# Kernel optimization log

Measured on AMD Instinct MI355X. Metric: run time of the kernel, lower is better.

The kernel has to match this reference:

```python
import jax, jax.numpy as jnp
import numpy as np

B, H, W = 8, 1024, 1024
DIM = 33  # LUT resolution per axis


def identity_lut(dim=DIM):
    # lut[0, b, g, r] = r/(dim-1); lut[1, b, g, r] = g/(dim-1); lut[2, b, g, r] = b/(dim-1)
    coords = jnp.arange(dim, dtype=jnp.float32) / (dim - 1)
    r = jnp.broadcast_to(coords[None, None, :], (dim, dim, dim))
    g = jnp.broadcast_to(coords[None, :, None], (dim, dim, dim))
    b = jnp.broadcast_to(coords[:, None, None], (dim, dim, dim))
    return jnp.stack([r, g, b], axis=0)  # [3, dim, dim, dim]


def setup_inputs() -> dict:
    key = jax.random.key(0)
    x = jax.random.uniform(key, (B, 3, H, W), dtype=jnp.float32)  # RGB in [0,1)
    lut = identity_lut(DIM)  # learned parameter, identity init as in the module
    return {"lut": lut, "x": x}


def _trilinear_lut_apply(lut, x):
    # lut: [3, dim, dim, dim] indexed as [channel, b, g, r]; x: [B, 3, H, W] in [0,1]
    dim = lut.shape[1]
    scale = jnp.float32(dim - 1)
    r = x[:, 0] * scale  # [B, H, W]
    g = x[:, 1] * scale
    b = x[:, 2] * scale

    ir = jnp.clip(jnp.floor(r).astype(jnp.int32), 0, dim - 2)
    ig = jnp.clip(jnp.floor(g).astype(jnp.int32), 0, dim - 2)
    ib = jnp.clip(jnp.floor(b).astype(jnp.int32), 0, dim - 2)

    fr = r - ir.astype(x.dtype)
    fg = g - ig.astype(x.dtype)
    fb = b - ib.astype(x.dtype)

    lut_flat = lut.reshape(3, dim * dim * dim)  # [3, dim^3]
    base = (ib * dim + ig) * dim + ir  # flat index of (b,g,r) corner, [B,H,W]

    out = jnp.zeros_like(x)  # [B, 3, H, W]
    for db in (0, 1):
        wb = fb if db else (1.0 - fb)
        for dg in (0, 1):
            wg = fg if dg else (1.0 - fg)
            for dr in (0, 1):
                wr = fr if dr else (1.0 - fr)
                idx = base + (db * dim + dg) * dim + dr  # [B,H,W]
                corner = lut_flat[:, idx]  # gather -> [3, B, H, W]
                w = (wb * wg * wr)[None]  # [1, B, H, W]
                out = out + jnp.transpose(corner * w, (1, 0, 2, 3))
    return out


def reference(lut, x):
    return _trilinear_lut_apply(lut, x)
```

## Files before the change

kernel.cpp:

```cpp
#include <hip/hip_runtime.h>
#include <math.h>

typedef float        f32x4 __attribute__((ext_vector_type(4)));
typedef unsigned int u32x4 __attribute__((ext_vector_type(4)));

static constexpr int DIM    = 33;
static constexpr int LUT_N  = DIM * DIM * DIM;
static constexpr int HW     = 1024 * 1024;
static constexpr int BATCH  = 8;
static constexpr long NPIX  = (long)BATCH * HW;
static constexpr long NTASK = NPIX / 4;

static constexpr size_t QT_BYTES  = (size_t)LUT_N * 4;
static constexpr size_t MM_OFF    = 143872;
static constexpr size_t LDS_BYTES = QT_BYTES;

static constexpr int ABLK = 256;
static constexpr int ATHR = 1024;

__device__ __forceinline__ f32x4 ntl4(const float* p) {
    return __builtin_nontemporal_load((const f32x4*)p);
}
__device__ __forceinline__ void nts4(float* p, f32x4 v) {
    __builtin_nontemporal_store(v, (f32x4*)p);
}
__device__ __forceinline__ float d_r(unsigned n) { return (float)(n & 1023u); }
__device__ __forceinline__ float d_g(unsigned n) { return (float)((n >> 10) & 1023u); }
__device__ __forceinline__ float d_b(unsigned n) { return (float)(n >> 20); }

__global__ __launch_bounds__(1024) void lut_minmax(
    const float* __restrict__ lut, float* __restrict__ mm) {
    __shared__ float smin[1024], smax[1024];
    int t = threadIdx.x;
    float vmin = 1e30f, vmax = -1e30f;
    const f32x4* l4 = (const f32x4*)lut;
    const int NV = (3 * LUT_N) / 4;
#pragma unroll 4
    for (int i = t; i < NV; i += 1024) {
        f32x4 v = l4[i];
        vmin = fminf(vmin, fminf(fminf(v[0], v[1]), fminf(v[2], v[3])));
        vmax = fmaxf(vmax, fmaxf(fmaxf(v[0], v[1]), fmaxf(v[2], v[3])));
    }
    if (t < 3) {
        float v = lut[NV * 4 + t];
        vmin = fminf(vmin, v);
        vmax = fmaxf(vmax, v);
    }
    smin[t] = vmin; smax[t] = vmax;
    __syncthreads();
    for (int s = 512; s > 0; s >>= 1) {
        if (t < s) {
            smin[t] = fminf(smin[t], smin[t + s]);
            smax[t] = fmaxf(smax[t], smax[t + s]);
        }
        __syncthreads();
    }
    if (t == 0) { mm[0] = smin[0]; mm[1] = smax[0]; }
}

__global__ __launch_bounds__(256) void repack_u10(
    const float* __restrict__ lut, unsigned* __restrict__ qt,
    const float* __restrict__ mm) {
    int i = blockIdx.x * 256 + threadIdx.x;
    if (i >= LUT_N) return;
    float mn = mm[0], mx = mm[1];
    float range = mx - mn;
    if (range < 1e-20f) range = 1e-20f;
    float scale = 1023.0f / range;
    unsigned qr = (unsigned)__float2int_rn((lut[i] - mn) * scale);
    unsigned qg = (unsigned)__float2int_rn((lut[LUT_N + i] - mn) * scale);
    unsigned qb = (unsigned)__float2int_rn((lut[2 * LUT_N + i] - mn) * scale);
    qt[i] = qr | (qg << 10) | (qb << 20);
}

__global__ __launch_bounds__(1024) void lut_apply_lds(
    const float* __restrict__ x, const unsigned* __restrict__ qt,
    const float* __restrict__ mm, float* __restrict__ out) {
    extern __shared__ unsigned sl[];
    {
        const u32x4* q4 = (const u32x4*)qt;
        u32x4* s4 = (u32x4*)sl;
#pragma unroll
        for (int k = 0; k < 9; ++k) {
            int i = threadIdx.x + k * 1024;
            if (i < LUT_N / 4) s4[i] = q4[i];
        }
        if (threadIdx.x == 0) sl[LUT_N - 1] = qt[LUT_N - 1];
    }
    float mn = mm[0];
    float range = mm[1] - mn;
    if (range < 1e-20f) range = 1e-20f;
    float inv = range * (1.0f / 1023.0f);
    __syncthreads();

    const int gtid = blockIdx.x * ATHR + threadIdx.x;
    const size_t hw4 = (size_t)gtid * 4;
    const float* xp = x + hw4;
    float*       op = out + hw4;

    f32x4 rc = ntl4(xp);
    f32x4 gc = ntl4(xp + HW);
    f32x4 bc = ntl4(xp + 2 * (size_t)HW);

    for (int it = 0; it < BATCH; ++it) {
        f32x4 rn = {}, gn = {}, bn = {};
        if (it != BATCH - 1) {
            const float* xn = xp + (size_t)(it + 1) * (3 * (size_t)HW);
            rn = ntl4(xn);
            gn = ntl4(xn + HW);
            bn = ntl4(xn + 2 * (size_t)HW);
        }

        unsigned n[4][8];
        float fr[4], fg[4], fb[4];
#pragma unroll
        for (int i = 0; i < 4; ++i) {
            const float scale = (float)(DIM - 1);
            float rs = rc[i] * scale, gs = gc[i] * scale, bs = bc[i] * scale;
            int ir = (int)rs; ir = ir < 0 ? 0 : (ir > DIM - 2 ? DIM - 2 : ir);
            int ig = (int)gs; ig = ig < 0 ? 0 : (ig > DIM - 2 ? DIM - 2 : ig);
            int ib = (int)bs; ib = ib < 0 ? 0 : (ib > DIM - 2 ? DIM - 2 : ib);
            fr[i] = rs - (float)ir;
            fg[i] = gs - (float)ig;
            fb[i] = bs - (float)ib;
            int s = ib * (DIM * DIM) + ig * DIM + ir;
            n[i][0] = sl[s];                     n[i][1] = sl[s + 1];
            n[i][2] = sl[s + DIM];               n[i][3] = sl[s + DIM + 1];
            n[i][4] = sl[s + DIM * DIM];         n[i][5] = sl[s + DIM * DIM + 1];
            n[i][6] = sl[s + DIM * DIM + DIM];   n[i][7] = sl[s + DIM * DIM + DIM + 1];
        }

        f32x4 orv, ogv, obv;
#pragma unroll
        for (int i = 0; i < 4; ++i) {
            float frc = 1.0f - fr[i], fgc = 1.0f - fg[i], fbc = 1.0f - fb[i];
            float w00 = fbc * fgc, w01 = fbc * fg[i];
            float w10 = fb[i] * fgc, w11 = fb[i] * fg[i];
            float u0 = w00 * frc, u1 = w00 * fr[i];
            float u2 = w01 * frc, u3 = w01 * fr[i];
            float u4 = w10 * frc, u5 = w10 * fr[i];
            float u6 = w11 * frc, u7 = w11 * fr[i];

            float qr = u0 * d_r(n[i][0]);
            qr = fmaf(u1, d_r(n[i][1]), qr);
            qr = fmaf(u2, d_r(n[i][2]), qr);
            qr = fmaf(u3, d_r(n[i][3]), qr);
            qr = fmaf(u4, d_r(n[i][4]), qr);
            qr = fmaf(u5, d_r(n[i][5]), qr);
            qr = fmaf(u6, d_r(n[i][6]), qr);
            qr = fmaf(u7, d_r(n[i][7]), qr);

            float qg = u0 * d_g(n[i][0]);
            qg = fmaf(u1, d_g(n[i][1]), qg);
            qg = fmaf(u2, d_g(n[i][2]), qg);
            qg = fmaf(u3, d_g(n[i][3]), qg);
            qg = fmaf(u4, d_g(n[i][4]), qg);
            qg = fmaf(u5, d_g(n[i][5]), qg);
            qg = fmaf(u6, d_g(n[i][6]), qg);
            qg = fmaf(u7, d_g(n[i][7]), qg);

            float qb = u0 * d_b(n[i][0]);
            qb = fmaf(u1, d_b(n[i][1]), qb);
            qb = fmaf(u2, d_b(n[i][2]), qb);
            qb = fmaf(u3, d_b(n[i][3]), qb);
            qb = fmaf(u4, d_b(n[i][4]), qb);
            qb = fmaf(u5, d_b(n[i][5]), qb);
            qb = fmaf(u6, d_b(n[i][6]), qb);
            qb = fmaf(u7, d_b(n[i][7]), qb);

            orv[i] = fmaf(qr, inv, mn);
            ogv[i] = fmaf(qg, inv, mn);
            obv[i] = fmaf(qb, inv, mn);
        }

        float* o = op + (size_t)it * (3 * (size_t)HW);
        nts4(o, orv);
        nts4(o + HW, ogv);
        nts4(o + 2 * (size_t)HW, obv);

        rc = rn; gc = gn; bc = bn;
    }
}

__global__ __launch_bounds__(256) void lut_apply_soa(
    const float* __restrict__ x, const float* __restrict__ lut,
    float* __restrict__ out) {
    long t = (long)blockIdx.x * 256 + threadIdx.x;
    long p = t * 4;
    int  b  = (int)(p >> 20);
    int  hw = (int)(p & (HW - 1));
    size_t base = (size_t)b * (3 * (size_t)HW) + (size_t)hw;

    float4 rv = *(const float4*)(x + base);
    float4 gv = *(const float4*)(x + base + (size_t)HW);
    float4 bv = *(const float4*)(x + base + 2 * (size_t)HW);

    float rr[4] = {rv.x, rv.y, rv.z, rv.w};
    float gg[4] = {gv.x, gv.y, gv.z, gv.w};
    float bb[4] = {bv.x, bv.y, bv.z, bv.w};
    float orr[4], org[4], orb[4];

#pragma unroll
    for (int i = 0; i < 4; ++i) {
        const float scale = (float)(DIM - 1);
        float rs = rr[i] * scale, gs = gg[i] * scale, bs = bb[i] * scale;
        int ir = (int)floorf(rs); ir = ir < 0 ? 0 : (ir > DIM - 2 ? DIM - 2 : ir);
        int ig = (int)floorf(gs); ig = ig < 0 ? 0 : (ig > DIM - 2 ? DIM - 2 : ig);
        int ib = (int)floorf(bs); ib = ib < 0 ? 0 : (ib > DIM - 2 ? DIM - 2 : ib);
        float fr = rs - (float)ir, fg = gs - (float)ig, fb = bs - (float)ib;
        int base_i = (ib * DIM + ig) * DIM + ir;
        float acc[3] = {0.f, 0.f, 0.f};
#pragma unroll
        for (int db = 0; db < 2; ++db) {
            float wb = db ? fb : 1.f - fb;
#pragma unroll
            for (int dg = 0; dg < 2; ++dg) {
                float wg = dg ? fg : 1.f - fg;
#pragma unroll
                for (int dr = 0; dr < 2; ++dr) {
                    float wr = dr ? fr : 1.f - fr;
                    int idx = base_i + (db * DIM + dg) * DIM + dr;
                    float w = wb * wg * wr;
                    acc[0] = fmaf(w, lut[idx], acc[0]);
                    acc[1] = fmaf(w, lut[LUT_N + idx], acc[1]);
                    acc[2] = fmaf(w, lut[2 * LUT_N + idx], acc[2]);
                }
            }
        }
        orr[i] = acc[0]; org[i] = acc[1]; orb[i] = acc[2];
    }

    *(float4*)(out + base)                  = make_float4(orr[0], orr[1], orr[2], orr[3]);
    *(float4*)(out + base + (size_t)HW)     = make_float4(org[0], org[1], org[2], org[3]);
    *(float4*)(out + base + 2 * (size_t)HW) = make_float4(orb[0], orb[1], orb[2], orb[3]);
}

extern "C" void kernel_launch(void* const* d_in, const int* in_sizes, int n_in,
                              void* d_out, int out_size, void* d_ws, size_t ws_size,
                              hipStream_t stream) {
    const float* lut = (const float*)d_in[0];
    const float* x   = (const float*)d_in[1];
    if (n_in >= 2 && in_sizes[0] > in_sizes[1]) {
        lut = (const float*)d_in[1];
        x   = (const float*)d_in[0];
    }
    float* out = (float*)d_out;

    const size_t need = MM_OFF + 2 * sizeof(float);
    if (ws_size >= need) {
        unsigned* qt = (unsigned*)d_ws;
        float*    mm = (float*)((char*)d_ws + MM_OFF);
        (void)hipFuncSetAttribute((const void*)lut_apply_lds,
                                  hipFuncAttributeMaxDynamicSharedMemorySize,
                                  (int)LDS_BYTES);
        lut_minmax<<<1, 1024, 0, stream>>>(lut, mm);
        repack_u10<<<(LUT_N + 255) / 256, 256, 0, stream>>>(lut, qt, mm);
        lut_apply_lds<<<ABLK, ATHR, LDS_BYTES, stream>>>(x, qt, mm, out);
    } else {
        lut_apply_soa<<<(int)(NTASK / 256), 256, 0, stream>>>(x, lut, out);
    }
}
```

Before: 189.3 us.

## Fuse LUT min/max, quantize-repack, and apply into a single kernel

```diff
diff --git a/kernel.cpp b/kernel.cpp
--- a/kernel.cpp
+++ b/kernel.cpp
@@ -12,8 +12,7 @@
 static constexpr long NTASK = NPIX / 4;
 
 static constexpr size_t QT_BYTES  = (size_t)LUT_N * 4;
-static constexpr size_t MM_OFF    = 143872;
-static constexpr size_t LDS_BYTES = QT_BYTES;
+static constexpr size_t LDS_BYTES = 143872;
 
 static constexpr int ABLK = 256;
 static constexpr int ATHR = 1024;
@@ -28,72 +27,59 @@
 __device__ __forceinline__ float d_g(unsigned n) { return (float)((n >> 10) & 1023u); }
 __device__ __forceinline__ float d_b(unsigned n) { return (float)(n >> 20); }
 
-__global__ __launch_bounds__(1024) void lut_minmax(
-    const float* __restrict__ lut, float* __restrict__ mm) {
-    __shared__ float smin[1024], smax[1024];
-    int t = threadIdx.x;
+__global__ __launch_bounds__(1024) void lut_fused(
+    const float* __restrict__ x, const float* __restrict__ lut,
+    float* __restrict__ out) {
+    extern __shared__ unsigned sl[];
+    const int t = threadIdx.x;
+
     float vmin = 1e30f, vmax = -1e30f;
-    const f32x4* l4 = (const f32x4*)lut;
-    const int NV = (3 * LUT_N) / 4;
+    {
+        const f32x4* l4 = (const f32x4*)lut;
+        const int NV = (3 * LUT_N) / 4;
 #pragma unroll 4
-    for (int i = t; i < NV; i += 1024) {
-        f32x4 v = l4[i];
-        vmin = fminf(vmin, fminf(fminf(v[0], v[1]), fminf(v[2], v[3])));
-        vmax = fmaxf(vmax, fmaxf(fmaxf(v[0], v[1]), fmaxf(v[2], v[3])));
-    }
-    if (t < 3) {
-        float v = lut[NV * 4 + t];
-        vmin = fminf(vmin, v);
-        vmax = fmaxf(vmax, v);
-    }
-    smin[t] = vmin; smax[t] = vmax;
+        for (int i = t; i < NV; i += 1024) {
+            f32x4 v = l4[i];
+            vmin = fminf(vmin, fminf(fminf(v[0], v[1]), fminf(v[2], v[3])));
+            vmax = fmaxf(vmax, fmaxf(fmaxf(v[0], v[1]), fmaxf(v[2], v[3])));
+        }
+        if (t < 3) {
+            float v = lut[NV * 4 + t];
+            vmin = fminf(vmin, v);
+            vmax = fmaxf(vmax, v);
+        }
+    }
+#pragma unroll
+    for (int off = 32; off > 0; off >>= 1) {
+        vmin = fminf(vmin, __shfl_down(vmin, off));
+        vmax = fmaxf(vmax, __shfl_down(vmax, off));
+    }
+    float* sf = (float*)sl;
+    if ((t & 63) == 0) { sf[t >> 6] = vmin; sf[16 + (t >> 6)] = vmax; }
     __syncthreads();
-    for (int s = 512; s > 0; s >>= 1) {
-        if (t < s) {
-            smin[t] = fminf(smin[t], smin[t + s]);
-            smax[t] = fmaxf(smax[t], smax[t + s]);
-        }
-        __syncthreads();
-    }
-    if (t == 0) { mm[0] = smin[0]; mm[1] = smax[0]; }
-}
-
-__global__ __launch_bounds__(256) void repack_u10(
-    const float* __restrict__ lut, unsigned* __restrict__ qt,
-    const float* __restrict__ mm) {
-    int i = blockIdx.x * 256 + threadIdx.x;
-    if (i >= LUT_N) return;
-    float mn = mm[0], mx = mm[1];
+    float mn = sf[0], mx = sf[16];
+#pragma unroll
+    for (int k = 1; k < 16; ++k) {
+        mn = fminf(mn, sf[k]);
+        mx = fmaxf(mx, sf[16 + k]);
+    }
+    __syncthreads();
+
     float range = mx - mn;
     if (range < 1e-20f) range = 1e-20f;
-    float scale = 1023.0f / range;
-    unsigned qr = (unsigned)__float2int_rn((lut[i] - mn) * scale);
-    unsigned qg = (unsigned)__float2int_rn((lut[LUT_N + i] - mn) * scale);
-    unsigned qb = (unsigned)__float2int_rn((lut[2 * LUT_N + i] - mn) * scale);
-    qt[i] = qr | (qg << 10) | (qb << 20);
-}
-
-__global__ __launch_bounds__(1024) void lut_apply_lds(
-    const float* __restrict__ x, const unsigned* __restrict__ qt,
-    const float* __restrict__ mm, float* __restrict__ out) {
-    extern __shared__ unsigned sl[];
-    {
-        const u32x4* q4 = (const u32x4*)qt;
-        u32x4* s4 = (u32x4*)sl;
-#pragma unroll
-        for (int k = 0; k < 9; ++k) {
-            int i = threadIdx.x + k * 1024;
-            if (i < LUT_N / 4) s4[i] = q4[i];
-        }
-        if (threadIdx.x == 0) sl[LUT_N - 1] = qt[LUT_N - 1];
-    }
-    float mn = mm[0];
-    float range = mm[1] - mn;
-    if (range < 1e-20f) range = 1e-20f;
-    float inv = range * (1.0f / 1023.0f);
+    const float qscale = 1023.0f / range;
+    const float inv    = range * (1.0f / 1023.0f);
+
+    for (int i = t; i < LUT_N; i += 1024) {
+        float r = lut[i], g = lut[LUT_N + i], b = lut[2 * LUT_N + i];
+        unsigned qr = (unsigned)__float2int_rn((r - mn) * qscale);
+        unsigned qg = (unsigned)__float2int_rn((g - mn) * qscale);
+        unsigned qb = (unsigned)__float2int_rn((b - mn) * qscale);
+        sl[i] = qr | (qg << 10) | (qb << 20);
+    }
     __syncthreads();
 
-    const int gtid = blockIdx.x * ATHR + threadIdx.x;
+    const int gtid = blockIdx.x * ATHR + t;
     const size_t hw4 = (size_t)gtid * 4;
     const float* xp = x + hw4;
     float*       op = out + hw4;
@@ -245,18 +231,10 @@
         x   = (const float*)d_in[0];
     }
     float* out = (float*)d_out;
-
-    const size_t need = MM_OFF + 2 * sizeof(float);
-    if (ws_size >= need) {
-        unsigned* qt = (unsigned*)d_ws;
-        float*    mm = (float*)((char*)d_ws + MM_OFF);
-        (void)hipFuncSetAttribute((const void*)lut_apply_lds,
-                                  hipFuncAttributeMaxDynamicSharedMemorySize,
-                                  (int)LDS_BYTES);
-        lut_minmax<<<1, 1024, 0, stream>>>(lut, mm);
-        repack_u10<<<(LUT_N + 255) / 256, 256, 0, stream>>>(lut, qt, mm);
-        lut_apply_lds<<<ABLK, ATHR, LDS_BYTES, stream>>>(x, qt, mm, out);
-    } else {
-        lut_apply_soa<<<(int)(NTASK / 256), 256, 0, stream>>>(x, lut, out);
-    }
-}
+    (void)d_ws; (void)ws_size;
+
+    (void)hipFuncSetAttribute((const void*)lut_fused,
+                              hipFuncAttributeMaxDynamicSharedMemorySize,
+                              (int)LDS_BYTES);
+    lut_fused<<<ABLK, ATHR, LDS_BYTES, stream>>>(x, lut, out);
+}
```

Result: no change. 188.6 us (-0.3%).
